# Kernel tuning notes

Measured on AMD Instinct MI355X. Metric: run time of the kernel, lower is better.

The kernel has to match this reference:

```python
import jax, jax.numpy as jnp
import numpy as np

jax.config.update("jax_enable_x64", True)

N = 3
NX = (N ** 2) ** 3          # 729 decision vars (flattened 9x9x9 one-hot board)
M2 = 128                    # dense inequality rows (G2)
QPEN = 0.1                  # Qpenalty -> Q = QPEN * I
NITER = 10                  # fixed interior-point iterations
SIGMA = 0.1                 # centering parameter
B = 16                      # batch of puzzles


def setup_inputs() -> dict:
    key = jax.random.key(0)
    k1, k2 = jax.random.split(key)
    puzzles = jax.random.uniform(k1, (B, 9, 9, 9), dtype=jnp.float32)
    G2 = jax.random.uniform(k2, (M2, NX), minval=-1.0, maxval=1.0, dtype=jnp.float32)
    z2 = jnp.zeros((NX,), jnp.float32)
    s2 = jnp.ones((M2,), jnp.float32)
    return {"puzzles": puzzles, "G2": G2, "z2": z2, "s2": s2}


def _qp_solve(p, G2, h):
    """Solve min 0.5 z'Qz + p'z  s.t. [-I; G2] z <= h for a batch of p.

    Primal-dual interior-point method, fixed NITER steps, exploiting the
    block structure G = [-I; G2]:  G' D G = diag(d1) + G2' D2 G2.
    p: (B, NX) float64. Returns z: (B, NX).
    """
    Bn, nx = p.shape
    G = jnp.concatenate([-jnp.eye(nx, dtype=p.dtype), G2], axis=0)  # (m, nx)
    m = G.shape[0]
    eye = jnp.eye(nx, dtype=p.dtype)

    z0 = jnp.zeros((Bn, nx), p.dtype)
    s0 = jnp.ones((Bn, m), p.dtype)
    lam0 = jnp.ones((Bn, m), p.dtype)

    def maxstep(x, dx):
        # largest alpha<=1 keeping x + alpha*dx > 0 (fraction-to-boundary 0.99)
        ratio = jnp.where(dx < 0, -x / jnp.where(dx < 0, dx, -1.0), jnp.inf)
        return jnp.minimum(1.0, 0.99 * jnp.min(ratio, axis=1))

    def step(carry, _):
        z, s, lam = carry
        Gz = z @ G.T                                   # (B, m)
        rd = QPEN * z + p + lam @ G                    # dual residual (B, nx)
        rp = Gz + s - h                                # primal residual (B, m)
        mu = jnp.mean(s * lam, axis=1, keepdims=True)  # (B, 1)
        d = lam / s                                    # (B, m)
        v = SIGMA * mu / s - lam + d * rp              # (B, m)
        rhs = -(rd + v @ G)                            # (B, nx)
        # K = Q + G' D G = diag(QPEN + d1) + G2' D2 G2  (block-sparse structure)
        K = jnp.einsum('mi,bm,mj->bij', G2, d[:, nx:], G2)
        K = K + eye[None] * (QPEN + d[:, :nx])[:, :, None]
        dz = jnp.linalg.solve(K, rhs[..., None])[..., 0]
        Gdz = dz @ G.T
        ds = -rp - Gdz
        dlam = v + d * Gdz
        alpha = jnp.minimum(maxstep(s, ds), maxstep(lam, dlam))[:, None]
        return (z + alpha * dz, s + alpha * ds, lam + alpha * dlam), None

    (z, _, _), _ = jax.lax.scan(step, (z0, s0, lam0), None, length=NITER)
    return z


def reference(puzzles, G2, z2, s2):
    Bn = puzzles.shape[0]
    G2d = G2.astype(jnp.float64)
    z2d = z2.astype(jnp.float64)
    s2d = s2.astype(jnp.float64)
    p = -puzzles.reshape(Bn, -1).astype(jnp.float64)     # (B, NX)
    h2 = G2d @ z2d + s2d                                 # (M2,)
    h = jnp.concatenate([jnp.zeros(NX, jnp.float64), h2])
    z = _qp_solve(p, G2d, h)
    return z.astype(jnp.float32).reshape(puzzles.shape)
```

## Files before the change

kernel.cpp:

```cpp
#include <hip/hip_runtime.h>
#include <math.h>

#define NXQ 729
#define M2Q 128
#define MQ  857
#define BQ  16
#define QPEN_ 0.1
#define SIGMA_ 0.1

typedef double d4 __attribute__((ext_vector_type(4)));

constexpr int OFF_P    = 0;
constexpr int OFF_H2   = OFF_P + BQ*NXQ;
constexpr int OFF_Q2   = OFF_H2 + M2Q;
constexpr int OFF_TP   = OFF_Q2 + BQ*M2Q;
constexpr int ST_Z    = 0;
constexpr int ST_S    = 729;
constexpr int ST_LAM  = 1586;
constexpr int ST_RP   = 2443;
constexpr int ST_V    = 3300;
constexpr int ST_AINV = 4157;
constexpr int ST_Y    = 4886;
constexpr int ST_GZ   = 5615;
constexpr int STB     = 5743;
constexpr int OFF_ST  = OFF_TP + 12*BQ*M2Q;
constexpr int SGB_B   = 20480;
constexpr int OFF_SG  = OFF_ST + 2*BQ*STB;

constexpr int L_SL   = 0;
constexpr int L_US   = 16512;
constexpr int L_INVD = 16640;
constexpr int L_RED2 = 16768;
constexpr int SH_FUSED = (16768 + 544) * 8;
constexpr int D_DZ   = 0;
constexpr int D_RED  = 736;
constexpr int D_SC   = 744;
constexpr int D_Q2   = 752;
constexpr int D_YL   = 880;
constexpr int D_SN   = 944;
constexpr int D_LN   = 1801;
constexpr int D_PART = 2658;
constexpr int D_AINV = 12672;
constexpr int AR_W   = 3168;
constexpr int SH_PS  = 12672 * 8;

__device__ __constant__ int TRI_R[10] = {0,1,1,2,2,2,3,3,3,3};
__device__ __constant__ int TRI_C[10] = {0,0,1,0,1,2,0,1,2,3};
__device__ __constant__ int TRL_R[28] = {0,1,1,2,2,2,3,3,3,3,4,4,4,4,4,5,5,5,5,5,5,6,6,6,6,6,6,6};
__device__ __constant__ int TRL_C[28] = {0,0,1,0,1,2,0,1,2,3,0,1,2,3,4,0,1,2,3,4,5,0,1,2,3,4,5,6};

__device__ __forceinline__ double wred_sum(double v) {
#pragma unroll
  for (int off = 32; off > 0; off >>= 1) v += __shfl_down(v, off, 64);
  return v;
}
__device__ __forceinline__ double wred_min(double v) {
#pragma unroll
  for (int off = 32; off > 0; off >>= 1) v = fmin(v, __shfl_down(v, off, 64));
  return v;
}
__device__ __forceinline__ double rsqrt64(double x) {
  double r = (double)rsqrtf((float)x);
  r = r * (1.5 - 0.5 * x * r * r);
  r = r * (1.5 - 0.5 * x * r * r);
  return r;
}

__device__ __forceinline__ void mfma_cdmap(int* rowm, int* colm) {
  const int lane = threadIdx.x & 63;
  const int rc = lane & 15, kq = lane >> 4;
  const double avr = (kq == 0) ? (double)rc : 0.0;
  const double bv1 = (kq == 0) ? 1.0 : 0.0;
  const double av1 = (kq == 0) ? 1.0 : 0.0;
  const double bvc = (kq == 0) ? (double)rc : 0.0;
  d4 zero = {0.0, 0.0, 0.0, 0.0};
  d4 dr = __builtin_amdgcn_mfma_f64_16x16x4f64(avr, bv1, zero, 0, 0, 0);
  d4 dc = __builtin_amdgcn_mfma_f64_16x16x4f64(av1, bvc, zero, 0, 0, 0);
#pragma unroll
  for (int e = 0; e < 4; ++e) { rowm[e] = (int)dr[e]; colm[e] = (int)dc[e]; }
}

__global__ __launch_bounds__(512)
void init_kernel(const float* __restrict__ puzzles, const float* __restrict__ G2,
                 const float* __restrict__ z2in, const float* __restrict__ s2in,
                 double* __restrict__ ws) {
  const int blk = blockIdx.x;
  const int tid = threadIdx.x, wave = tid >> 6, lane = tid & 63;
  __shared__ double sm[32];
  if (blk < BQ) {
    const int bb = blk;
    double* st = ws + OFF_ST + bb * STB;
    for (int i = tid; i < NXQ; i += 512) {
      ws[OFF_P + bb * NXQ + i] = -(double)puzzles[bb * NXQ + i];
      st[ST_Z + i] = 0.0;
      st[ST_AINV + i] = 1.0 / (QPEN_ + 1.0);
      st[ST_RP + i] = 1.0;
      st[ST_V + i] = SIGMA_;
    }
    for (int i = tid; i < MQ; i += 512) { st[ST_S + i] = 1.0; st[ST_LAM + i] = 1.0; }
    if (tid < M2Q) st[ST_GZ + tid] = 0.0;
  } else {
    const int r = blk - 16;
    double acc = 0.0;
    for (int kx = tid; kx < NXQ; kx += 512)
      acc += (double)G2[r * NXQ + kx] * (double)z2in[kx];
    acc = wred_sum(acc);
    if (lane == 0) sm[wave] = acc;
    __syncthreads();
    if (tid == 0) {
      double t = 0.0;
#pragma unroll
      for (int w = 0; w < 8; ++w) t += sm[w];
      const double h2r = t + (double)s2in[r];
      ws[OFF_H2 + r] = h2r;
      sm[16] = h2r;
    }
    __syncthreads();
    if (tid < BQ) {
      double* st = ws + OFF_ST + tid * STB;
      const double rp2 = 1.0 - sm[16];
      st[ST_RP + NXQ + r] = rp2;
      st[ST_V  + NXQ + r] = rp2 - 0.9;
      ws[OFF_Q2 + tid * M2Q + r] = rp2 + 0.1;
    }
  }
}

__device__ __forceinline__ void sbuild_half(const float* __restrict__ G2,
                                            const double* __restrict__ ainv,
                                            double* __restrict__ arena,
                                            double* __restrict__ Sgb,
                                            const int tile, const int half,
                                            const int* rowm, const int* colm) {
  const int tid = threadIdx.x, wave = tid >> 6, lane = tid & 63;
  const int R0 = TRI_R[tile] * 32, C0 = TRI_C[tile] * 32;
  double* As = arena + wave * AR_W;
  double* Bs = As + 1584;
  const int kw0 = half * 368 + wave * 92;
  const int kwend = min(kw0 + 92, NXQ);
  const int kk16 = lane & 15, rsub = lane >> 4;
  const int rc = lane & 15, kq = lane >> 4;
  d4 c00 = {0.0, 0.0, 0.0, 0.0}, c01 = c00, c10 = c00, c11 = c00;
  float pa[24], pb[24];
  if (wave < 4) {
#pragma unroll
    for (int it = 0; it < 24; ++it) {
      const int kk = (it >> 3) * 16 + kk16;
      const int rr = (it & 7) * 4 + rsub;
      const int k = kw0 + kk;
      const int kc = (k < kwend) ? k : (kwend - 1);
      pa[it] = G2[(R0 + rr) * NXQ + kc];
      pb[it] = G2[(C0 + rr) * NXQ + kc];
    }
  }
  for (int ch = 0; ch < 2; ++ch) {
    __syncthreads();
    if (wave < 4) {
#pragma unroll
      for (int it = 0; it < 24; ++it) {
        const int kk = (it >> 3) * 16 + kk16;
        const int rr = (it & 7) * 4 + rsub;
        const int k = kw0 + ch * 48 + kk;
        const bool ok = (k < kwend);
        const double aik = ok ? ainv[k] : 0.0;
        As[kk * 33 + rr] = ok ? (double)pa[it] * aik : 0.0;
        Bs[kk * 33 + rr] = ok ? (double)pb[it] : 0.0;
      }
      if (ch == 0) {
#pragma unroll
        for (int it = 0; it < 24; ++it) {
          const int kk = (it >> 3) * 16 + kk16;
          const int rr = (it & 7) * 4 + rsub;
          const int k = kw0 + 48 + kk;
          const int kc = (k < kwend) ? k : (kwend - 1);
          pa[it] = G2[(R0 + rr) * NXQ + kc];
          pb[it] = G2[(C0 + rr) * NXQ + kc];
        }
      }
    }
    __syncthreads();
    if (wave < 4) {
#pragma unroll
      for (int s = 0; s < 12; ++s) {
        const int ko = (s * 4 + kq) * 33;
        const double a0 = As[ko + rc],      a1 = As[ko + 16 + rc];
        const double b0 = Bs[ko + rc],      b1 = Bs[ko + 16 + rc];
        c00 = __builtin_amdgcn_mfma_f64_16x16x4f64(a0, b0, c00, 0, 0, 0);
        c01 = __builtin_amdgcn_mfma_f64_16x16x4f64(a0, b1, c01, 0, 0, 0);
        c10 = __builtin_amdgcn_mfma_f64_16x16x4f64(a1, b0, c10, 0, 0, 0);
        c11 = __builtin_amdgcn_mfma_f64_16x16x4f64(a1, b1, c11, 0, 0, 0);
      }
    }
  }
  __syncthreads();
  if (wave < 4) {
#pragma unroll
    for (int e = 0; e < 4; ++e) {
      As[rowm[e] * 33 + colm[e]]              = c00[e];
      As[rowm[e] * 33 + 16 + colm[e]]         = c01[e];
      As[(16 + rowm[e]) * 33 + colm[e]]       = c10[e];
      As[(16 + rowm[e]) * 33 + 16 + colm[e]]  = c11[e];
    }
  }
  __syncthreads();
  for (int idx = tid; idx < 1024; idx += 512) {
    const int r = idx >> 5, c = idx & 31;
    const int o = r * 33 + c;
    const double v = arena[o] + arena[AR_W + o] + arena[2*AR_W + o] + arena[3*AR_W + o];
    Sgb[(tile * 2 + half) * 1024 + idx] = v;
  }
}

__device__ __forceinline__ void run_sbuild_units(const float* __restrict__ G2,
                                                 const double* __restrict__ ainv,
                                                 double* __restrict__ arena,
                                                 double* __restrict__ Sgb,
                                                 const int y,
                                                 const int* rowm, const int* colm) {
  if (y < 12) {
    sbuild_half(G2, ainv, arena, Sgb, y >> 1, y & 1, rowm, colm);
  } else {
    const int u0 = 12 + (y - 12) * 2;
    sbuild_half(G2, ainv, arena, Sgb, u0 >> 1, u0 & 1, rowm, colm);
    sbuild_half(G2, ainv, arena, Sgb, (u0 + 1) >> 1, (u0 + 1) & 1, rowm, colm);
  }
}

__global__ __launch_bounds__(512)
void ps_kernel(const float* __restrict__ G2, double* __restrict__ ws) {
  const int b = blockIdx.x, tile = blockIdx.y;
  const int tid = threadIdx.x, lane = tid & 63;
  extern __shared__ double sm[];
  double* st = ws + OFF_ST + b * STB;
  if (tile < 12) {
    double* uvec = sm;
    double* part = sm + 128;
    double* yl   = sm + 640;
    const int c0 = tile * 64;
    if (tid < M2Q) uvec[tid] = ws[OFF_Q2 + b * M2Q + tid];
    __syncthreads();
    const int kk = tid & 63, rq = tid >> 6;
    const int k = c0 + kk;
    const int kg = (k < NXQ) ? k : (NXQ - 1);
    {
      const float* gp = G2 + (rq * 16) * NXQ + kg;
      double acc = 0.0;
#pragma unroll
      for (int j = 0; j < 16; ++j) acc = fma((double)gp[j * NXQ], uvec[rq * 16 + j], acc);
      part[rq * 64 + kk] = acc;
    }
    __syncthreads();
    if (tid < 64) {
      const int k2 = c0 + tid;
      double y = 0.0;
      if (k2 < NXQ) {
        double w = 0.0;
#pragma unroll
        for (int q = 0; q < 8; ++q) w += part[q * 64 + tid];
        const double rhsk = -(QPEN_ * st[ST_Z + k2] + ws[OFF_P + b * NXQ + k2]
                              - st[ST_LAM + k2] - st[ST_V + k2] + w);
        y = st[ST_AINV + k2] * rhsk;
        st[ST_Y + k2] = y;
      }
      yl[tid] = y;
    }
    __syncthreads();
    {
      const double yv = yl[lane];
      double pp[16];
#pragma unroll
      for (int jr = 0; jr < 16; ++jr)
        pp[jr] = (double)G2[((tid >> 6) * 16 + jr) * NXQ + kg] * yv;
#pragma unroll
      for (int st2 = 0; st2 < 4; ++st2) {
        const int m = 32 >> st2, half = 8 >> st2;
        const bool hi = (lane & m) != 0;
#pragma unroll
        for (int r = 0; r < 8; ++r) {
          if (r < half) {
            const double send = hi ? pp[r] : pp[r + half];
            const double recv = __shfl_xor(send, m, 64);
            pp[r] = (hi ? pp[r + half] : pp[r]) + recv;
          }
        }
      }
      double tot = pp[0];
      tot += __shfl_xor(tot, 2, 64);
      tot += __shfl_xor(tot, 1, 64);
      if ((lane & 3) == 0)
        ws[OFF_TP + (tile * BQ + b) * M2Q + (tid >> 6) * 16 + ((lane >> 2) & 15)] = tot;
    }
    __syncthreads();
  }
  {
    int rowm[4], colm[4];
    mfma_cdmap(rowm, colm);
    run_sbuild_units(G2, st + ST_AINV, sm, ws + OFF_SG + b * SGB_B, tile,
                     rowm, colm);
  }
}

__global__ __launch_bounds__(512, 1)
void dps_kernel(const float* __restrict__ G2, double* __restrict__ ws,
                float* __restrict__ out, const int ph, const int last) {
  const int b = blockIdx.x, chunk = blockIdx.y;
  const int tid = threadIdx.x, wave = tid >> 6, lane = tid & 63;
  extern __shared__ double sm[];
  double (*Sl)[129] = (double(*)[129])(sm + L_SL);
  double* us   = sm + L_US;
  double* invd = sm + L_INVD;
  double* red2 = sm + L_RED2;
  const double* R = ws + OFF_ST + ph * BQ * STB + b * STB;
  double*       W = ws + OFF_ST + (1 - ph) * BQ * STB + b * STB;
  double* Sgb  = ws + OFF_SG + b * SGB_B;
  const int c0 = chunk * 64;

#pragma unroll
  for (int t = 0; t < 10; ++t) {
    const int R0 = TRI_R[t] * 32, C0 = TRI_C[t] * 32;
    for (int e = tid; e < 1024; e += 512) {
      const int r = e >> 5, c = e & 31;
      Sl[R0 + r][C0 + c] = Sgb[(t * 2) * 1024 + e] + Sgb[(t * 2 + 1) * 1024 + e];
    }
  }
  if (tid < M2Q) {
    double t = 0.0;
#pragma unroll
    for (int c = 0; c < 12; ++c) t += ws[OFF_TP + (c * BQ + b) * M2Q + tid];
    us[tid] = t;
  }
  __syncthreads();
  if (tid < M2Q) Sl[tid][tid] += R[ST_S + NXQ + tid] / R[ST_LAM + NXQ + tid];
  __syncthreads();

  int rowm[4], colm[4];
  mfma_cdmap(rowm, colm);
  const int rc16 = lane & 15, kq4 = lane >> 4;

  auto panel16 = [&](const int K0) {
    const int r = lane;
    double a[16];
#pragma unroll
    for (int c = 0; c < 16; ++c) a[c] = Sl[K0 + r][K0 + c];
#pragma unroll
    for (int c = 0; c < 16; ++c) {
      const double dcc = __shfl(a[c], c, 64);
      const double rs = rsqrt64(dcc);
      a[c] *= rs;
      if (lane == c) invd[K0 + c] = rs;
#pragma unroll
      for (int k2 = c + 1; k2 < 16; ++k2) {
        const double lkc = __shfl(a[c], k2, 64);
        a[k2] = fma(-a[c], lkc, a[k2]);
      }
    }
#pragma unroll
    for (int c = 0; c < 16; ++c) Sl[K0 + r][K0 + c] = a[c];
  };

  auto tile_upd = [&](const int K0, const int i0, const int j0) {
    d4 tacc;
#pragma unroll
    for (int e = 0; e < 4; ++e) tacc[e] = Sl[i0 + rowm[e]][j0 + colm[e]];
#pragma unroll
    for (int m = 0; m < 4; ++m) {
      const double av = -Sl[i0 + rc16][K0 + 4 * m + kq4];
      const double bv =  Sl[j0 + rc16][K0 + 4 * m + kq4];
      tacc = __builtin_amdgcn_mfma_f64_16x16x4f64(av, bv, tacc, 0, 0, 0);
    }
#pragma unroll
    for (int e = 0; e < 4; ++e) Sl[i0 + rowm[e]][j0 + colm[e]] = tacc[e];
  };

  if (wave == 0 && lane < 16) panel16(0);
  __syncthreads();

  for (int kb = 0; kb < 8; ++kb) {
    const int K0 = kb * 16, J0 = K0 + 16, T = 128 - J0;
    if (tid <= T) {
      const bool isU = (tid == T);
      double l[16];
      if (isU) {
#pragma unroll
        for (int c = 0; c < 16; ++c) l[c] = us[K0 + c];
      } else {
#pragma unroll
        for (int c = 0; c < 16; ++c) l[c] = Sl[J0 + tid][K0 + c];
      }
#pragma unroll
      for (int c = 0; c < 16; ++c) {
        const double lc = l[c] * invd[K0 + c];
        l[c] = lc;
#pragma unroll
        for (int k2 = c + 1; k2 < 16; ++k2)
          l[k2] = fma(-lc, Sl[K0 + k2][K0 + c], l[k2]);
      }
      if (isU) {
#pragma unroll
        for (int c = 0; c < 16; ++c) us[K0 + c] = l[c];
      } else {
#pragma unroll
        for (int c = 0; c < 16; ++c) Sl[J0 + tid][K0 + c] = l[c];
      }
    }
    __syncthreads();

    if (kb < 7) {
      if (tid < T) {
        double acc = 0.0;
#pragma unroll
        for (int c = 0; c < 16; ++c) acc = fma(Sl[J0 + tid][K0 + c], us[K0 + c], acc);
        us[J0 + tid] -= acc;
      }
      if (wave == 7) tile_upd(K0, J0, J0);
      __syncthreads();
      const int Tb = 7 - kb;
      const int nt = (Tb * (Tb + 1)) >> 1;
      if (wave == 0) {
        if (lane < 16) panel16(J0);
      } else {
        for (int idx = wave; idx < nt; idx += 7)
          tile_upd(K0, J0 + TRL_R[idx] * 16, J0 + TRL_C[idx] * 16);
      }
      __syncthreads();
    }
  }

  for (int kb = 7; kb >= 0; --kb) {
    const int K0 = kb * 16;
    if (kb < 7) {
      const int c = tid & 15, ch = tid >> 4;
      double part = 0.0;
      for (int k = K0 + 16 + ch; k < 128; k += 32) part = fma(Sl[k][K0 + c], us[k], part);
      red2[ch * 17 + c] = part;
    }
    __syncthreads();
    if (wave == 0 && lane < 16) {
      const int j = lane;
      double x = us[K0 + j];
      if (kb < 7) {
        double acc = 0.0;
#pragma unroll
        for (int q = 0; q < 32; ++q) acc += red2[q * 17 + j];
        x -= acc;
      }
      double colv[16];
#pragma unroll
      for (int c = 0; c < 16; ++c) colv[c] = Sl[K0 + c][K0 + j];
      const double iv = invd[K0 + j];
#pragma unroll
      for (int cc = 0; cc < 16; ++cc) {
        const int c = 15 - cc;
        const double xiv = x * iv;
        const double uc = __shfl(xiv, c, 64);
        if (j == c) x = xiv;
        else if (j < c) x = fma(-colv[c], uc, x);
      }
      us[K0 + j] = x;
    }
    __syncthreads();
  }
  if (tid < M2Q) invd[tid] = (R[ST_S + NXQ + tid] / R[ST_LAM + NXQ + tid]) * us[tid];
  __syncthreads();
  double* g2b = invd;

  double* dzl   = sm + D_DZ;
  double* red   = sm + D_RED;
  double* sc    = sm + D_SC;
  double* ainvn = sm + D_AINV;
  double* q2l   = sm + D_Q2;
  double* yl    = sm + D_YL;
  double* snew  = sm + D_SN;
  double* lnew  = sm + D_LN;
  double* part  = sm + D_PART;

  double lmin = 1e300;
  for (int k = tid; k < NXQ; k += 512) {
    double accv = 0.0;
    const float* gp = G2 + k;
#pragma unroll 16
    for (int r = 0; r < M2Q; ++r) accv = fma((double)gp[r * NXQ], us[r], accv);
    const double dzv = R[ST_Y + k] - R[ST_AINV + k] * accv;
    dzl[k] = dzv;
    const double si = R[ST_S + k], li = R[ST_LAM + k], di = li / si;
    const double dsi = dzv - R[ST_RP + k];
    const double dlami = R[ST_V + k] - di * dzv;
    snew[k] = dsi; lnew[k] = dlami;
    if (dsi < 0.0)   lmin = fmin(lmin, -si / dsi);
    if (dlami < 0.0) lmin = fmin(lmin, -li / dlami);
  }
  if (tid < M2Q) {
    const int i = NXQ + tid;
    const double si = R[ST_S + i], li = R[ST_LAM + i], di = li / si;
    const double g = g2b[tid];
    const double dsi = -R[ST_RP + i] - g;
    const double dlami = R[ST_V + i] + di * g;
    snew[i] = dsi; lnew[i] = dlami;
    if (dsi < 0.0)   lmin = fmin(lmin, -si / dsi);
    if (dlami < 0.0) lmin = fmin(lmin, -li / dlami);
  }
  lmin = wred_min(lmin);
  if (lane == 0) red[wave] = lmin;
  __syncthreads();
  if (tid == 0) {
    double m = red[0];
#pragma unroll
    for (int w = 1; w < 8; ++w) m = fmin(m, red[w]);
    sc[0] = fmin(1.0, 0.99 * m);
  }
  __syncthreads();
  const double alpha = sc[0];

  if (last) {
    const int k2 = c0 + (tid & 63);
    if (tid < 64 && k2 < NXQ)
      out[b * NXQ + k2] = (float)(R[ST_Z + k2] + alpha * dzl[k2]);
    return;
  }

  double musum = 0.0;
  for (int i = tid; i < MQ; i += 512) {
    const double si = R[ST_S + i], li = R[ST_LAM + i];
    const double sn = si + alpha * snew[i], ln = li + alpha * lnew[i];
    snew[i] = sn; lnew[i] = ln;
    musum += sn * ln;
  }
  musum = wred_sum(musum);
  if (lane == 0) red[wave] = musum;
  __syncthreads();
  if (tid == 0) {
    double t = 0.0;
#pragma unroll
    for (int w = 0; w < 8; ++w) t += red[w];
    sc[1] = SIGMA_ * (t / (double)MQ);
  }
  __syncthreads();
  const double smu = sc[1];

  for (int i = tid; i < MQ; i += 512) {
    const double sn = snew[i], ln = lnew[i], di = ln / sn;
    if (i < NXQ) {
      const double zn = R[ST_Z + i] + alpha * dzl[i];
      const double rpn = sn - zn;
      const double vn = smu / sn - ln + di * rpn;
      const double an = 1.0 / (QPEN_ + di);
      ainvn[i] = an;
      if ((i >> 6) == chunk) {
        W[ST_Z + i] = zn; W[ST_S + i] = sn; W[ST_LAM + i] = ln;
        W[ST_RP + i] = rpn; W[ST_V + i] = vn; W[ST_AINV + i] = an;
      }
    } else {
      const int m = i - NXQ;
      const double gzn = R[ST_GZ + m] + alpha * g2b[m];
      const double rpn = gzn + sn - ws[OFF_H2 + m];
      const double vn = smu / sn - ln + di * rpn;
      q2l[m] = ln + vn;
      if (chunk == 0) {
        W[ST_S + i] = sn; W[ST_LAM + i] = ln;
        W[ST_RP + i] = rpn; W[ST_V + i] = vn; W[ST_GZ + m] = gzn;
      }
    }
  }
  __syncthreads();

  if (chunk < 12) {
    const int kk = tid & 63, rq = tid >> 6;
    const int k = c0 + kk;
    const int kg = (k < NXQ) ? k : (NXQ - 1);
    {
      const float* gp = G2 + (rq * 16) * NXQ + kg;
      double acc = 0.0;
#pragma unroll
      for (int j = 0; j < 16; ++j) acc = fma((double)gp[j * NXQ], q2l[rq * 16 + j], acc);
      part[rq * 64 + kk] = acc;
    }
    __syncthreads();
    if (tid < 64) {
      const int k2 = c0 + tid;
      double y = 0.0;
      if (k2 < NXQ) {
        double w = 0.0;
#pragma unroll
        for (int q = 0; q < 8; ++q) w += part[q * 64 + tid];
        const double sn = snew[k2], ln = lnew[k2], di = ln / sn;
        const double zn = R[ST_Z + k2] + alpha * dzl[k2];
        const double rpn = sn - zn;
        const double vn = smu / sn - ln + di * rpn;
        const double rhsk = -(QPEN_ * zn + ws[OFF_P + b * NXQ + k2] - ln - vn + w);
        y = ainvn[k2] * rhsk;
        W[ST_Y + k2] = y;
      }
      yl[tid] = y;
    }
    __syncthreads();
    {
      const double yv = yl[lane];
      double pp[16];
#pragma unroll
      for (int jr = 0; jr < 16; ++jr)
        pp[jr] = (double)G2[((tid >> 6) * 16 + jr) * NXQ + kg] * yv;
#pragma unroll
      for (int st2 = 0; st2 < 4; ++st2) {
        const int m = 32 >> st2, half = 8 >> st2;
        const bool hi = (lane & m) != 0;
#pragma unroll
        for (int r = 0; r < 8; ++r) {
          if (r < half) {
            const double send = hi ? pp[r] : pp[r + half];
            const double recv = __shfl_xor(send, m, 64);
            pp[r] = (hi ? pp[r + half] : pp[r]) + recv;
          }
        }
      }
      double tot = pp[0];
      tot += __shfl_xor(tot, 2, 64);
      tot += __shfl_xor(tot, 1, 64);
      if ((lane & 3) == 0)
        ws[OFF_TP + (chunk * BQ + b) * M2Q + (tid >> 6) * 16 + ((lane >> 2) & 15)] = tot;
    }
    __syncthreads();
  }

  run_sbuild_units(G2, ainvn, sm, Sgb, chunk, rowm, colm);
}

extern "C" void kernel_launch(void* const* d_in, const int* in_sizes, int n_in,
                              void* d_out, int out_size, void* d_ws, size_t ws_size,
                              hipStream_t stream) {
  const float* puzzles = (const float*)d_in[0];
  const float* G2      = (const float*)d_in[1];
  const float* z2      = (const float*)d_in[2];
  const float* s2      = (const float*)d_in[3];
  float* out = (float*)d_out;
  double* ws = (double*)d_ws;

  (void)hipFuncSetAttribute(reinterpret_cast<const void*>(&dps_kernel),
                            hipFuncAttributeMaxDynamicSharedMemorySize, SH_FUSED);
  (void)hipFuncSetAttribute(reinterpret_cast<const void*>(&ps_kernel),
                            hipFuncAttributeMaxDynamicSharedMemorySize, SH_PS);

  init_kernel<<<dim3(16 + M2Q), dim3(512), 0, stream>>>(puzzles, G2, z2, s2, ws);
  ps_kernel<<<dim3(BQ, 16), dim3(512), SH_PS, stream>>>(G2, ws);
  for (int it = 0; it < 10; ++it) {
    const int ph = it & 1;
    dps_kernel<<<dim3(BQ, 16), dim3(512), SH_FUSED, stream>>>(G2, ws, out, ph, (it == 9) ? 1 : 0);
  }
}
```

Before: 829.5 us.

## Build each S tile in one block using all eight waves over K

The G2' D G2 tile construction previously split each of the 10 lower-triangular 32x32 tiles into two K-halves across blocks, with only 4 waves per block doing MFMA work. Now each tile is built by a single block whose 8 waves each take a 92-wide K slice, processed in 16-wide chunks without block barriers, and reduced across 8 wave partials. The half-sum in the consumer goes away, and the diagonal s/lam term is folded into the tile load, removing a barrier. The trade-off is that the S-build work moves onto blocks y>=6 only, so per-block work on those blocks grows, and the G2-row tail is moved to the last waves.

```diff
diff --git a/kernel.cpp b/kernel.cpp
--- a/kernel.cpp
+++ b/kernel.cpp
@@ -24,7 +24,7 @@
 constexpr int ST_GZ   = 5615;
 constexpr int STB     = 5743;
 constexpr int OFF_ST  = OFF_TP + 12*BQ*M2Q;
-constexpr int SGB_B   = 20480;
+constexpr int SGB_B   = 10240;
 constexpr int OFF_SG  = OFF_ST + 2*BQ*STB;
 
 constexpr int L_SL   = 0;
@@ -41,8 +41,8 @@
 constexpr int D_LN   = 1801;
 constexpr int D_PART = 2658;
 constexpr int D_AINV = 12672;
-constexpr int AR_W   = 3168;
-constexpr int SH_PS  = 12672 * 8;
+constexpr int AR_W   = 1056;
+constexpr int SH_PS  = 8448 * 8;
 
 __device__ __constant__ int TRI_R[10] = {0,1,1,2,2,2,3,3,3,3};
 __device__ __constant__ int TRI_C[10] = {0,0,1,0,1,2,0,1,2,3};
@@ -126,117 +126,94 @@
   }
 }
 
-__device__ __forceinline__ void sbuild_half(const float* __restrict__ G2,
-                                            const double* __restrict__ ainv,
-                                            double* __restrict__ arena,
-                                            double* __restrict__ Sgb,
-                                            const int tile, const int half,
-                                            const int* rowm, const int* colm) {
+__device__ __forceinline__ void sbuild_tile8(const float* __restrict__ G2,
+                                             const double* __restrict__ ainv,
+                                             double* __restrict__ arena,
+                                             double* __restrict__ Sgb, const int tile,
+                                             const int* rowm, const int* colm) {
   const int tid = threadIdx.x, wave = tid >> 6, lane = tid & 63;
   const int R0 = TRI_R[tile] * 32, C0 = TRI_C[tile] * 32;
   double* As = arena + wave * AR_W;
-  double* Bs = As + 1584;
-  const int kw0 = half * 368 + wave * 92;
+  double* Bs = As + 528;
+  const int kw0 = wave * 92;
   const int kwend = min(kw0 + 92, NXQ);
   const int kk16 = lane & 15, rsub = lane >> 4;
   const int rc = lane & 15, kq = lane >> 4;
   d4 c00 = {0.0, 0.0, 0.0, 0.0}, c01 = c00, c10 = c00, c11 = c00;
-  float pa[24], pb[24];
-  if (wave < 4) {
-#pragma unroll
-    for (int it = 0; it < 24; ++it) {
-      const int kk = (it >> 3) * 16 + kk16;
-      const int rr = (it & 7) * 4 + rsub;
-      const int k = kw0 + kk;
-      const int kc = (k < kwend) ? k : (kwend - 1);
+  float pa[8], pb[8];
+  {
+    const int k = kw0 + kk16;
+    const int kc = (k < kwend) ? k : (kwend - 1);
+#pragma unroll
+    for (int it = 0; it < 8; ++it) {
+      const int rr = it * 4 + rsub;
       pa[it] = G2[(R0 + rr) * NXQ + kc];
       pb[it] = G2[(C0 + rr) * NXQ + kc];
     }
   }
-  for (int ch = 0; ch < 2; ++ch) {
-    __syncthreads();
-    if (wave < 4) {
-#pragma unroll
-      for (int it = 0; it < 24; ++it) {
-        const int kk = (it >> 3) * 16 + kk16;
-        const int rr = (it & 7) * 4 + rsub;
-        const int k = kw0 + ch * 48 + kk;
-        const bool ok = (k < kwend);
-        const double aik = ok ? ainv[k] : 0.0;
-        As[kk * 33 + rr] = ok ? (double)pa[it] * aik : 0.0;
-        Bs[kk * 33 + rr] = ok ? (double)pb[it] : 0.0;
-      }
-      if (ch == 0) {
-#pragma unroll
-        for (int it = 0; it < 24; ++it) {
-          const int kk = (it >> 3) * 16 + kk16;
-          const int rr = (it & 7) * 4 + rsub;
-          const int k = kw0 + 48 + kk;
-          const int kc = (k < kwend) ? k : (kwend - 1);
-          pa[it] = G2[(R0 + rr) * NXQ + kc];
-          pb[it] = G2[(C0 + rr) * NXQ + kc];
-        }
-      }
-    }
-    __syncthreads();
-    if (wave < 4) {
-#pragma unroll
-      for (int s = 0; s < 12; ++s) {
-        const int ko = (s * 4 + kq) * 33;
-        const double a0 = As[ko + rc],      a1 = As[ko + 16 + rc];
-        const double b0 = Bs[ko + rc],      b1 = Bs[ko + 16 + rc];
-        c00 = __builtin_amdgcn_mfma_f64_16x16x4f64(a0, b0, c00, 0, 0, 0);
-        c01 = __builtin_amdgcn_mfma_f64_16x16x4f64(a0, b1, c01, 0, 0, 0);
-        c10 = __builtin_amdgcn_mfma_f64_16x16x4f64(a1, b0, c10, 0, 0, 0);
-        c11 = __builtin_amdgcn_mfma_f64_16x16x4f64(a1, b1, c11, 0, 0, 0);
-      }
-    }
-  }
-  __syncthreads();
-  if (wave < 4) {
-#pragma unroll
-    for (int e = 0; e < 4; ++e) {
-      As[rowm[e] * 33 + colm[e]]              = c00[e];
-      As[rowm[e] * 33 + 16 + colm[e]]         = c01[e];
-      As[(16 + rowm[e]) * 33 + colm[e]]       = c10[e];
-      As[(16 + rowm[e]) * 33 + 16 + colm[e]]  = c11[e];
-    }
+  for (int ch = 0; ch < 6; ++ch) {
+    {
+      const int k = kw0 + ch * 16 + kk16;
+      const bool ok = (k < kwend);
+      const double aik = ok ? ainv[k] : 0.0;
+#pragma unroll
+      for (int it = 0; it < 8; ++it) {
+        const int rr = it * 4 + rsub;
+        As[kk16 * 33 + rr] = ok ? (double)pa[it] * aik : 0.0;
+        Bs[kk16 * 33 + rr] = ok ? (double)pb[it] : 0.0;
+      }
+    }
+    if (ch < 5) {
+      const int k = kw0 + (ch + 1) * 16 + kk16;
+      const int kc = (k < kwend) ? k : (kwend - 1);
+#pragma unroll
+      for (int it = 0; it < 8; ++it) {
+        const int rr = it * 4 + rsub;
+        pa[it] = G2[(R0 + rr) * NXQ + kc];
+        pb[it] = G2[(C0 + rr) * NXQ + kc];
+      }
+    }
+#pragma unroll
+    for (int s = 0; s < 4; ++s) {
+      const int ko = (s * 4 + kq) * 33;
+      const double a0 = As[ko + rc], a1 = As[ko + 16 + rc];
+      const double b0 = Bs[ko + rc], b1 = Bs[ko + 16 + rc];
+      c00 = __builtin_amdgcn_mfma_f64_16x16x4f64(a0, b0, c00, 0, 0, 0);
+      c01 = __builtin_amdgcn_mfma_f64_16x16x4f64(a0, b1, c01, 0, 0, 0);
+      c10 = __builtin_amdgcn_mfma_f64_16x16x4f64(a1, b0, c10, 0, 0, 0);
+      c11 = __builtin_amdgcn_mfma_f64_16x16x4f64(a1, b1, c11, 0, 0, 0);
+    }
+  }
+  double* Wp = arena + wave * AR_W;
+#pragma unroll
+  for (int e = 0; e < 4; ++e) {
+    Wp[rowm[e] * 33 + colm[e]]             = c00[e];
+    Wp[rowm[e] * 33 + 16 + colm[e]]        = c01[e];
+    Wp[(16 + rowm[e]) * 33 + colm[e]]      = c10[e];
+    Wp[(16 + rowm[e]) * 33 + 16 + colm[e]] = c11[e];
   }
   __syncthreads();
   for (int idx = tid; idx < 1024; idx += 512) {
     const int r = idx >> 5, c = idx & 31;
     const int o = r * 33 + c;
-    const double v = arena[o] + arena[AR_W + o] + arena[2*AR_W + o] + arena[3*AR_W + o];
-    Sgb[(tile * 2 + half) * 1024 + idx] = v;
-  }
-}
-
-__device__ __forceinline__ void run_sbuild_units(const float* __restrict__ G2,
-                                                 const double* __restrict__ ainv,
-                                                 double* __restrict__ arena,
-                                                 double* __restrict__ Sgb,
-                                                 const int y,
-                                                 const int* rowm, const int* colm) {
-  if (y < 12) {
-    sbuild_half(G2, ainv, arena, Sgb, y >> 1, y & 1, rowm, colm);
-  } else {
-    const int u0 = 12 + (y - 12) * 2;
-    sbuild_half(G2, ainv, arena, Sgb, u0 >> 1, u0 & 1, rowm, colm);
-    sbuild_half(G2, ainv, arena, Sgb, (u0 + 1) >> 1, (u0 + 1) & 1, rowm, colm);
+    double v = arena[o];
+#pragma unroll
+    for (int w = 1; w < 8; ++w) v += arena[w * AR_W + o];
+    Sgb[tile * 1024 + idx] = v;
   }
 }
 
 __global__ __launch_bounds__(512)
 void ps_kernel(const float* __restrict__ G2, double* __restrict__ ws) {
-  const int b = blockIdx.x, tile = blockIdx.y;
+  const int b = blockIdx.x, y = blockIdx.y;
   const int tid = threadIdx.x, lane = tid & 63;
   extern __shared__ double sm[];
   double* st = ws + OFF_ST + b * STB;
-  if (tile < 12) {
+  if (y < 12) {
     double* uvec = sm;
     double* part = sm + 128;
     double* yl   = sm + 640;
-    const int c0 = tile * 64;
+    const int c0 = y * 64;
     if (tid < M2Q) uvec[tid] = ws[OFF_Q2 + b * M2Q + tid];
     __syncthreads();
     const int kk = tid & 63, rq = tid >> 6;
@@ -252,17 +229,17 @@
     __syncthreads();
     if (tid < 64) {
       const int k2 = c0 + tid;
-      double y = 0.0;
+      double yv = 0.0;
       if (k2 < NXQ) {
         double w = 0.0;
 #pragma unroll
         for (int q = 0; q < 8; ++q) w += part[q * 64 + tid];
         const double rhsk = -(QPEN_ * st[ST_Z + k2] + ws[OFF_P + b * NXQ + k2]
                               - st[ST_LAM + k2] - st[ST_V + k2] + w);
-        y = st[ST_AINV + k2] * rhsk;
-        st[ST_Y + k2] = y;
-      }
-      yl[tid] = y;
+        yv = st[ST_AINV + k2] * rhsk;
+        st[ST_Y + k2] = yv;
+      }
+      yl[tid] = yv;
     }
     __syncthreads();
     {
@@ -288,15 +265,15 @@
       tot += __shfl_xor(tot, 2, 64);
       tot += __shfl_xor(tot, 1, 64);
       if ((lane & 3) == 0)
-        ws[OFF_TP + (tile * BQ + b) * M2Q + (tid >> 6) * 16 + ((lane >> 2) & 15)] = tot;
-    }
-    __syncthreads();
-  }
-  {
+        ws[OFF_TP + (y * BQ + b) * M2Q + (tid >> 6) * 16 + ((lane >> 2) & 15)] = tot;
+    }
+    __syncthreads();
+  }
+  if (y >= 6) {
     int rowm[4], colm[4];
     mfma_cdmap(rowm, colm);
-    run_sbuild_units(G2, st + ST_AINV, sm, ws + OFF_SG + b * SGB_B, tile,
-                     rowm, colm);
+    sbuild_tile8(G2, st + ST_AINV, sm, ws + OFF_SG + b * SGB_B, y - 6,
+                 rowm, colm);
   }
 }
 
@@ -318,9 +295,15 @@
 #pragma unroll
   for (int t = 0; t < 10; ++t) {
     const int R0 = TRI_R[t] * 32, C0 = TRI_C[t] * 32;
+    const bool dg = (R0 == C0);
     for (int e = tid; e < 1024; e += 512) {
       const int r = e >> 5, c = e & 31;
-      Sl[R0 + r][C0 + c] = Sgb[(t * 2) * 1024 + e] + Sgb[(t * 2 + 1) * 1024 + e];
+      double v = Sgb[t * 1024 + e];
+      if (dg && r == c) {
+        const int i = C0 + c;
+        v += R[ST_S + NXQ + i] / R[ST_LAM + NXQ + i];
+      }
+      Sl[R0 + r][C0 + c] = v;
     }
   }
   if (tid < M2Q) {
@@ -329,8 +312,6 @@
     for (int c = 0; c < 12; ++c) t += ws[OFF_TP + (c * BQ + b) * M2Q + tid];
     us[tid] = t;
   }
-  __syncthreads();
-  if (tid < M2Q) Sl[tid][tid] += R[ST_S + NXQ + tid] / R[ST_LAM + NXQ + tid];
   __syncthreads();
 
   int rowm[4], colm[4];
@@ -489,10 +470,11 @@
     if (dsi < 0.0)   lmin = fmin(lmin, -si / dsi);
     if (dlami < 0.0) lmin = fmin(lmin, -li / dlami);
   }
-  if (tid < M2Q) {
-    const int i = NXQ + tid;
+  if (tid >= 384) {
+    const int m = tid - 384;
+    const int i = NXQ + m;
     const double si = R[ST_S + i], li = R[ST_LAM + i], di = li / si;
-    const double g = g2b[tid];
+    const double g = g2b[m];
     const double dsi = -R[ST_RP + i] - g;
     const double dlami = R[ST_V + i] + di * g;
     snew[i] = dsi; lnew[i] = dlami;
@@ -621,7 +603,8 @@
     __syncthreads();
   }
 
-  run_sbuild_units(G2, ainvn, sm, Sgb, chunk, rowm, colm);
+  if (chunk >= 6)
+    sbuild_tile8(G2, ainvn, sm, Sgb, chunk - 6, rowm, colm);
 }
 
 extern "C" void kernel_launch(void* const* d_in, const int* in_sizes, int n_in,
```

Result: no change. 832.7 us (+0.4%).
